# Kernel optimization log

Hardware: AMD Instinct MI355X
Metric: run time of the kernel (lower is better)

Reference implementation:

```python
import jax, jax.numpy as jnp
import numpy as np

IOU_THRES = 0.45
NEG_POS_RATIO = 3
BBOX_XFORM_CLIP = float(np.log(1000.0 / 16.0))  # torchvision BoxCoder clamp


def _make_boxes(key, shape, img=512.0):
    # valid xyxy boxes inside a 512x512 image
    k1, k2 = jax.random.split(key)
    cxy = jax.random.uniform(k1, shape + (2,), minval=32.0, maxval=img - 32.0)
    wh = jax.random.uniform(k2, shape + (2,), minval=8.0, maxval=128.0)
    return jnp.concatenate([cxy - 0.5 * wh, cxy + 0.5 * wh], axis=-1)


def setup_inputs() -> dict:
    key = jax.random.key(0)
    B, A, G, C = 32, 32768, 64, 91
    ks = jax.random.split(key, 5)
    return {
        "cls_logits": jax.random.normal(ks[0], (B, A, C), dtype=jnp.float32),
        "bbox_regression": 0.1 * jax.random.normal(ks[1], (B, A, 4), dtype=jnp.float32),
        "anchors": _make_boxes(ks[2], (B, A)),
        "gt_boxes": _make_boxes(ks[3], (B, G)),
        "gt_labels": jax.random.randint(ks[4], (B, G), 0, C - 1),  # fg classes; C-1 is background
    }


def _pairwise_iou(boxes, anchors):
    # boxes [B,G,4] xyxy, anchors [B,A,4] xyxy -> [B,G,A]
    b = boxes[:, :, None, :]
    a = anchors[:, None, :, :]
    tl = jnp.maximum(b[..., :2], a[..., :2])
    br = jnp.minimum(b[..., 2:], a[..., 2:])
    wh = jnp.clip(br - tl, 0.0)
    inter = wh[..., 0] * wh[..., 1]
    area_b = (b[..., 2] - b[..., 0]) * (b[..., 3] - b[..., 1])
    area_a = (a[..., 2] - a[..., 0]) * (a[..., 3] - a[..., 1])
    return inter / (area_b + area_a - inter + 1e-16)


def _match(ious):
    # SSDMatcher: per-anchor best gt, threshold, then force best anchor per gt.
    # ious [G,A] -> matches [A] in {-1, 0..G-1}
    G = ious.shape[0]
    vals = ious.max(axis=0)
    m = jnp.argmax(ious, axis=0)
    m = jnp.where(vals < IOU_THRES, -1, m)
    best_anchor_per_gt = jnp.argmax(ious, axis=1)  # [G]
    return m.at[best_anchor_per_gt].set(jnp.arange(G))


def _decode(reg, anchors):
    # torchvision BoxCoder.decode_single, weights (1,1,1,1), xyxy anchors
    w = anchors[..., 2] - anchors[..., 0]
    h = anchors[..., 3] - anchors[..., 1]
    cx = anchors[..., 0] + 0.5 * w
    cy = anchors[..., 1] + 0.5 * h
    dx, dy, dw, dh = reg[..., 0], reg[..., 1], reg[..., 2], reg[..., 3]
    dw = jnp.minimum(dw, BBOX_XFORM_CLIP)
    dh = jnp.minimum(dh, BBOX_XFORM_CLIP)
    pcx = dx * w + cx
    pcy = dy * h + cy
    pw = jnp.exp(dw) * w
    ph = jnp.exp(dh) * h
    return jnp.stack([pcx - 0.5 * pw, pcy - 0.5 * ph, pcx + 0.5 * pw, pcy + 0.5 * ph], axis=-1)


def _giou_loss(pred, gt):
    # GIoU loss on xyxy boxes; elementwise over leading dims
    tl = jnp.maximum(pred[..., :2], gt[..., :2])
    br = jnp.minimum(pred[..., 2:], gt[..., 2:])
    wh = jnp.clip(br - tl, 0.0)
    inter = wh[..., 0] * wh[..., 1]
    ap = (pred[..., 2] - pred[..., 0]) * (pred[..., 3] - pred[..., 1])
    ag = (gt[..., 2] - gt[..., 0]) * (gt[..., 3] - gt[..., 1])
    union = ap + ag - inter + 1e-16
    iou = inter / union
    ctl = jnp.minimum(pred[..., :2], gt[..., :2])
    cbr = jnp.maximum(pred[..., 2:], gt[..., 2:])
    cwh = cbr - ctl
    ac = cwh[..., 0] * cwh[..., 1]
    giou = iou - (ac - union) / jnp.clip(ac, 1e-16)
    return 1.0 - jnp.clip(giou, -1.0, 1.0)


def reference(cls_logits, bbox_regression, anchors, gt_boxes, gt_labels):
    B, A, C = cls_logits.shape
    # --- matching ---
    ious = _pairwise_iou(gt_boxes, anchors)        # [B,G,A]
    matched = jax.vmap(_match)(ious)               # [B,A]
    fg = matched >= 0                              # [B,A]
    idx = jnp.clip(matched, 0)
    num_fg = fg.sum()
    # --- bbox loss (sum over foreground only, via masking) ---
    matched_gt = jnp.take_along_axis(gt_boxes, idx[..., None], axis=1)  # [B,A,4]
    pred = _decode(bbox_regression, anchors)                            # [B,A,4]
    bbox_loss_sum = jnp.sum(_giou_loss(pred, matched_gt) * fg)
    # --- classification targets + CE ---
    matched_lbl = jnp.take_along_axis(gt_labels, idx, axis=1)           # [B,A]
    cls_targets = jnp.where(fg, matched_lbl, C - 1)
    logp = jax.nn.log_softmax(cls_logits, axis=-1)
    cls_loss = -jnp.take_along_axis(logp, cls_targets[..., None], axis=-1)[..., 0]  # [B,A]
    neg_loss = jnp.where(fg, -jnp.inf, cls_loss)
    order = jnp.argsort(-neg_loss, axis=1)         # descending
    rank = jnp.argsort(order, axis=1)
    num_neg = NEG_POS_RATIO * fg.sum(axis=1, keepdims=True)
    bg = rank < num_neg
    # --- normalize ---
    N = jnp.maximum(1, num_fg).astype(cls_loss.dtype)
    bbox_loss = 2.0 * bbox_loss_sum / N
    cls_total = (jnp.sum(cls_loss * fg) + jnp.sum(cls_loss * bg)) / N
    return jnp.stack([bbox_loss, cls_total])  # [bbox_loss, cls_loss]
```

## Files before the change

### kernel.cpp

```cpp
#include <hip/hip_runtime.h>
#include <hip/hip_bf16.h>

#define B 32
#define A 32768
#define G 64
#define C 91
#define NBINS 2048

typedef unsigned long long ull;

static constexpr size_t offMatched = 0;
static constexpr size_t offLoss    = (size_t)B * A * 4;
static constexpr size_t offHist    = (size_t)2 * B * A * 4;
static constexpr size_t offNumFg   = offHist + (size_t)B * NBINS * 4;
static constexpr size_t offPrefix  = offNumFg + B * 4;
static constexpr size_t offKrem    = offPrefix + B * 4;
static constexpr size_t offDone    = offKrem + B * 4;
static constexpr size_t offT       = offDone + B * 4;
static constexpr size_t offR       = offT + B * 4;
static constexpr size_t offAcc     = offR + B * 4;
static constexpr size_t offGt      = offAcc + 3 * 8;
static constexpr int    ZERO_N     = (int)((offGt - offHist) / 4);

__global__ void init_kernel(int* zero_base, ull* gtpack) {
  int i = blockIdx.x * 256 + threadIdx.x;
  for (int j = i; j < ZERO_N; j += gridDim.x * 256) zero_base[j] = 0;
  if (i < B * G) gtpack[i] = 0xFFFFFFFFull;
}

__global__ __launch_bounds__(256) void match_kernel(
    const float4* __restrict__ anchors, const float4* __restrict__ gt_boxes,
    int* __restrict__ matched, ull* __restrict__ gtpack) {
#pragma clang fp contract(off)
  int b = blockIdx.y;
  int a = blockIdx.x * 256 + threadIdx.x;
  __shared__ float4 gtb[G];
  __shared__ float gtarea[G];
  __shared__ ull best[G];
  if (threadIdx.x < G) {
    float4 g = gt_boxes[b * G + threadIdx.x];
    gtb[threadIdx.x] = g;
    gtarea[threadIdx.x] = (g.z - g.x) * (g.w - g.y);
    best[threadIdx.x] = 0ull;
  }
  __syncthreads();
  float4 an = anchors[(size_t)b * A + a];
  float area_a = (an.z - an.x) * (an.w - an.y);
  float bestv = -1.0f;
  int bestg = 0;
  for (int g = 0; g < G; ++g) {
    float4 gb = gtb[g];
    float tlx = fmaxf(gb.x, an.x), tly = fmaxf(gb.y, an.y);
    float brx = fminf(gb.z, an.z), bry = fminf(gb.w, an.w);
    float w = fmaxf(brx - tlx, 0.0f), h = fmaxf(bry - tly, 0.0f);
    float inter = w * h;
    float iou = 0.0f;
    if (inter > 0.0f) iou = inter / (gtarea[g] + area_a - inter + 1e-16f);
    if (iou > bestv) { bestv = iou; bestg = g; }
    if (iou > 0.0f) {
      ull p = ((ull)__float_as_uint(iou) << 32) | (unsigned)(~(unsigned)a);
      if (p > best[g]) atomicMax(&best[g], p);
    }
  }
  matched[(size_t)b * A + a] = (bestv < 0.45f) ? -1 : bestg;
  __syncthreads();
  if (threadIdx.x < G) {
    ull p = best[threadIdx.x];
    if (p) atomicMax(&gtpack[b * G + threadIdx.x], p);
  }
}

__global__ void force_kernel(const ull* __restrict__ gtpack, int* __restrict__ matched) {
  int b = blockIdx.x * blockDim.x + threadIdx.x;
  if (b < B) {
    for (int g = 0; g < G; ++g) {
      unsigned a = ~(unsigned)(gtpack[b * G + g] & 0xFFFFFFFFull);
      matched[(size_t)b * A + a] = g;
    }
  }
}

#define APB 64
#define NT 8
#define NF4 (APB * C / 4)
#define NSTG 6
#define TAILN (NF4 - (NSTG - 1) * 256)

__device__ __forceinline__ void stage_tile(const float4* src, float* dst, int tid) {
  int wbase = tid & ~63;
#pragma unroll
  for (int r = 0; r < NSTG - 1; ++r)
    __builtin_amdgcn_global_load_lds(
        (const __attribute__((address_space(1))) void*)(src + r * 256 + tid),
        (__attribute__((address_space(3))) void*)(dst + (r * 256 + wbase) * 4),
        16, 0, 0);
  if (tid < TAILN)
    __builtin_amdgcn_global_load_lds(
        (const __attribute__((address_space(1))) void*)(src + (NSTG - 1) * 256 + tid),
        (__attribute__((address_space(3))) void*)(dst + ((NSTG - 1) * 256 + wbase) * 4),
        16, 0, 0);
}

__global__ __launch_bounds__(256) void loss_kernel(
    const float4* __restrict__ logit4, const float4* __restrict__ reg,
    const float4* __restrict__ anchors, const float4* __restrict__ gt_boxes,
    const int* __restrict__ gt_labels, const int* __restrict__ matched,
    float* __restrict__ cls_loss, int* __restrict__ num_fg, double* __restrict__ acc) {
  __shared__ float buf[2][APB * C];
  __shared__ double rb[4], rf[4];
  __shared__ int rc[4];
  int tid = threadIdx.x;
  int b = blockIdx.y;
  int tile0 = blockIdx.x * NT;
  size_t bbase4 = (size_t)b * A * C / 4;
  int t4 = tid >> 2, q = tid & 3;

  stage_tile(logit4 + bbase4 + (size_t)tile0 * NF4, buf[0], tid);
  int mmCur = matched[(size_t)b * A + tile0 * APB + t4];
  int tclsCur = (mmCur >= 0) ? gt_labels[b * G + mmCur] : (C - 1);
  __syncthreads();

  double bbs = 0.0, fgs = 0.0;
  int cnt = 0;

  for (int t = 0; t < NT; ++t) {
    int cur = t & 1;
    if (t + 1 < NT)
      stage_tile(logit4 + bbase4 + (size_t)(tile0 + t + 1) * NF4, buf[cur ^ 1], tid);
    int mmNext = 0, tclsNext = 0;
    if (t + 1 < NT) {
      mmNext = matched[(size_t)b * A + (tile0 + t + 1) * APB + t4];
      tclsNext = (mmNext >= 0) ? gt_labels[b * G + mmNext] : (C - 1);
    }
    {
      const float* BC = buf[cur];
      int a = (tile0 + t) * APB + t4;
      const float* row = BC + t4 * C + 23 * q;
      const int cn = (q < 3) ? 23 : 22;
      float s0 = 0.f, s1 = 0.f, s2 = 0.f, s3 = 0.f;
      int j = 0;
#pragma unroll
      for (; j + 4 <= 20; j += 4) {
        s0 += __expf(row[j]);
        s1 += __expf(row[j + 1]);
        s2 += __expf(row[j + 2]);
        s3 += __expf(row[j + 3]);
      }
      for (; j < cn; ++j) s0 += __expf(row[j]);
      float s = (s0 + s1) + (s2 + s3);
      s += __shfl_xor(s, 1);
      s += __shfl_xor(s, 2);
      float lse = __logf(s);
      float xt = BC[t4 * C + tclsCur];
      float loss = lse - xt;
      if (q == 0) {
        cls_loss[(size_t)b * A + a] = loss;
        if (mmCur >= 0) {
          fgs += (double)loss;
          cnt++;
          float4 an = anchors[(size_t)b * A + a];
          float4 rg = reg[(size_t)b * A + a];
          float4 gb = gt_boxes[b * G + mmCur];
          float w = an.z - an.x, h = an.w - an.y;
          float cx = an.x + 0.5f * w, cy = an.y + 0.5f * h;
          float dw = fminf(rg.z, 4.135166556742356f);
          float dh = fminf(rg.w, 4.135166556742356f);
          float pcx = rg.x * w + cx, pcy = rg.y * h + cy;
          float pw = expf(dw) * w, ph = expf(dh) * h;
          float px0 = pcx - 0.5f * pw, py0 = pcy - 0.5f * ph;
          float px1 = pcx + 0.5f * pw, py1 = pcy + 0.5f * ph;
          float tlx = fmaxf(px0, gb.x), tly = fmaxf(py0, gb.y);
          float brx = fminf(px1, gb.z), bry = fminf(py1, gb.w);
          float iw = fmaxf(brx - tlx, 0.f), ih = fmaxf(bry - tly, 0.f);
          float inter = iw * ih;
          float ap = (px1 - px0) * (py1 - py0);
          float ag = (gb.z - gb.x) * (gb.w - gb.y);
          float uni = ap + ag - inter + 1e-16f;
          float iou = inter / uni;
          float ctlx = fminf(px0, gb.x), ctly = fminf(py0, gb.y);
          float cbrx = fmaxf(px1, gb.z), cbry = fmaxf(py1, gb.w);
          float acr = (cbrx - ctlx) * (cbry - ctly);
          float giou = iou - (acr - uni) / fmaxf(acr, 1e-16f);
          giou = fminf(fmaxf(giou, -1.f), 1.f);
          bbs += (double)(1.f - giou);
        }
      }
    }
    mmCur = mmNext;
    tclsCur = tclsNext;
    __syncthreads();
  }

  int lane = tid & 63, wave = tid >> 6;
  for (int off = 32; off; off >>= 1) {
    bbs += __shfl_xor(bbs, off);
    fgs += __shfl_xor(fgs, off);
    cnt += __shfl_xor(cnt, off);
  }
  if (lane == 0) { rb[wave] = bbs; rf[wave] = fgs; rc[wave] = cnt; }
  __syncthreads();
  if (tid == 0) {
    double tb = rb[0] + rb[1] + rb[2] + rb[3];
    double tf = rf[0] + rf[1] + rf[2] + rf[3];
    int tc = rc[0] + rc[1] + rc[2] + rc[3];
    if (tb != 0.0) atomicAdd(&acc[0], tb);
    if (tf != 0.0) atomicAdd(&acc[1], tf);
    if (tc) atomicAdd(&num_fg[b], tc);
  }
}

__global__ __launch_bounds__(256) void hist_kernel(
    const float* __restrict__ cls_loss, const int* __restrict__ matched,
    int* __restrict__ hist, const int* __restrict__ done,
    const unsigned* __restrict__ prefix, int level) {
  int b = blockIdx.y;
  if (level > 1 && done[b]) return;
  __shared__ int h[NBINS];
  for (int i = threadIdx.x; i < NBINS; i += 256) h[i] = 0;
  __syncthreads();
  unsigned pref = (level > 1) ? prefix[b] : 0u;
  int base = blockIdx.x * 2048;
  for (int i = 0; i < 8; ++i) {
    int a = base + i * 256 + threadIdx.x;
    if (matched[(size_t)b * A + a] < 0) {
      unsigned bits = __float_as_uint(cls_loss[(size_t)b * A + a]);
      if (level == 1) atomicAdd(&h[bits >> 21], 1);
      else if (level == 2) { if ((bits >> 21) == pref) atomicAdd(&h[(bits >> 10) & 2047], 1); }
      else { if ((bits >> 10) == pref) atomicAdd(&h[bits & 1023], 1); }
    }
  }
  __syncthreads();
  for (int i = threadIdx.x; i < NBINS; i += 256)
    if (h[i]) atomicAdd(&hist[b * NBINS + i], h[i]);
}

__global__ __launch_bounds__(256) void select_kernel(
    int* __restrict__ hist, const int* __restrict__ num_fg, int* __restrict__ done,
    unsigned* __restrict__ prefix, int* __restrict__ krem, float* __restrict__ T,
    int* __restrict__ r, double* __restrict__ acc, int level) {
  int b = blockIdx.x;
  if (level > 1 && done[b]) return;
  int nb = (level == 3) ? 1024 : 2048;
  int per = nb / 256;
  __shared__ int h[NBINS];
  __shared__ int gsum[256];
  for (int i = threadIdx.x; i < nb; i += 256) {
    h[i] = hist[b * NBINS + i];
    hist[b * NBINS + i] = 0;
  }
  __syncthreads();
  int gs = 0;
  for (int j = 0; j < per; ++j) gs += h[threadIdx.x * per + j];
  gsum[threadIdx.x] = gs;
  __syncthreads();
  if (threadIdx.x == 0) {
    int k;
    bool dn = false;
    if (level == 1) {
      int nf = num_fg[b];
      k = 3 * nf;
      int bgcnt = A - nf;
      if (k <= 0) { T[b] = __builtin_inff(); r[b] = 0; done[b] = 1; dn = true; }
      else if (k >= bgcnt) { T[b] = -1.0f; r[b] = 0; done[b] = 1; dn = true; }
    } else {
      k = krem[b];
    }
    if (!dn) {
      int run = 0, gidx = 255;
      for (; gidx >= 0; --gidx) {
        if (run + gsum[gidx] >= k) break;
        run += gsum[gidx];
      }
      if (gidx < 0) {
        T[b] = -1.0f; r[b] = 0; done[b] = 1;
      } else {
        int bin = gidx * per + per - 1;
        for (; bin > gidx * per; --bin) {
          if (run + h[bin] >= k) break;
          run += h[bin];
        }
        int kn = k - run;
        if (level == 1) { prefix[b] = (unsigned)bin; krem[b] = kn; }
        else if (level == 2) { prefix[b] = (prefix[b] << 11) | (unsigned)bin; krem[b] = kn; }
        else {
          unsigned bits = (prefix[b] << 10) | (unsigned)bin;
          float t = __uint_as_float(bits);
          T[b] = t; r[b] = kn;
          if (kn > 0) atomicAdd(&acc[2], (double)kn * (double)t);
        }
      }
    }
  }
}

__global__ __launch_bounds__(256) void bgsum_kernel(
    const float* __restrict__ cls_loss, const int* __restrict__ matched,
    const float* __restrict__ T, double* __restrict__ acc) {
  int b = blockIdx.y;
  float t = T[b];
  float local = 0.f;
  int base = blockIdx.x * 2048;
  for (int i = 0; i < 8; ++i) {
    int a = base + i * 256 + threadIdx.x;
    if (matched[(size_t)b * A + a] < 0) {
      float v = cls_loss[(size_t)b * A + a];
      if (v > t) local += v;
    }
  }
  for (int off = 32; off; off >>= 1) local += __shfl_xor(local, off);
  __shared__ double sd[4];
  if ((threadIdx.x & 63) == 0) sd[threadIdx.x >> 6] = (double)local;
  __syncthreads();
  if (threadIdx.x == 0) {
    double tt = sd[0] + sd[1] + sd[2] + sd[3];
    if (tt != 0.0) atomicAdd(&acc[2], tt);
  }
}

__global__ void finalize_kernel(const int* __restrict__ num_fg,
                                const double* __restrict__ acc, float* __restrict__ out) {
  if (threadIdx.x == 0 && blockIdx.x == 0) {
    int tot = 0;
    for (int b = 0; b < B; ++b) tot += num_fg[b];
    double N = (double)(tot > 1 ? tot : 1);
    out[0] = (float)(2.0 * acc[0] / N);
    out[1] = (float)((acc[1] + acc[2]) / N);
  }
}

extern "C" void kernel_launch(void* const* d_in, const int* in_sizes, int n_in,
                              void* d_out, int out_size, void* d_ws, size_t ws_size,
                              hipStream_t stream) {
  const float4* logit4  = (const float4*)d_in[0];
  const float4* reg     = (const float4*)d_in[1];
  const float4* anchors = (const float4*)d_in[2];
  const float4* gtb     = (const float4*)d_in[3];
  const int*    gtl     = (const int*)d_in[4];

  char* ws = (char*)d_ws;
  int*      matched = (int*)(ws + offMatched);
  float*    closs   = (float*)(ws + offLoss);
  int*      hist    = (int*)(ws + offHist);
  int*      numfg   = (int*)(ws + offNumFg);
  unsigned* prefix  = (unsigned*)(ws + offPrefix);
  int*      krem    = (int*)(ws + offKrem);
  int*      done    = (int*)(ws + offDone);
  float*    T       = (float*)(ws + offT);
  int*      r       = (int*)(ws + offR);
  double*   acc     = (double*)(ws + offAcc);
  ull*      gtpack  = (ull*)(ws + offGt);
  float*    out     = (float*)d_out;

  init_kernel<<<64, 256, 0, stream>>>((int*)(ws + offHist), gtpack);
  match_kernel<<<dim3(A / 256, B), 256, 0, stream>>>(anchors, gtb, matched, gtpack);
  force_kernel<<<1, 64, 0, stream>>>(gtpack, matched);
  loss_kernel<<<dim3(A / (APB * NT), B), 256, 0, stream>>>(
      logit4, reg, anchors, gtb, gtl, matched, closs, numfg, acc);
  hist_kernel<<<dim3(A / 2048, B), 256, 0, stream>>>(closs, matched, hist, done, prefix, 1);
  select_kernel<<<B, 256, 0, stream>>>(hist, numfg, done, prefix, krem, T, r, acc, 1);
  hist_kernel<<<dim3(A / 2048, B), 256, 0, stream>>>(closs, matched, hist, done, prefix, 2);
  select_kernel<<<B, 256, 0, stream>>>(hist, numfg, done, prefix, krem, T, r, acc, 2);
  hist_kernel<<<dim3(A / 2048, B), 256, 0, stream>>>(closs, matched, hist, done, prefix, 3);
  select_kernel<<<B, 256, 0, stream>>>(hist, numfg, done, prefix, krem, T, r, acc, 3);
  bgsum_kernel<<<dim3(A / 2048, B), 256, 0, stream>>>(closs, matched, T, acc);
  finalize_kernel<<<1, 64, 0, stream>>>(numfg, acc, out);
}
```

Baseline: 730.3 us.

## Fuse radix-select passes into one per-image kernel and fold the force and finalize steps

Replaces the three histogram and select kernel pairs, the background sum and the finalize kernel with a single kernel using one 1024-thread block per image. Each block holds all of that image's loss bits in registers and runs three radix histogram levels in shared memory. The forced-match step moves into the last match block, and finalize into the last select block, both coordinated by atomic tickets. The loss kernel now writes masked bits (zero for foreground), so the selection passes no longer re-read the match array. This trims kernel launches and global re-reads, in exchange for only 32 blocks in the select phase and reliance on threadfence and ticket ordering.

```diff
diff --git a/kernel.cpp b/kernel.cpp
--- a/kernel.cpp
+++ b/kernel.cpp
@@ -10,33 +10,29 @@
 typedef unsigned long long ull;
 
 static constexpr size_t offMatched = 0;
-static constexpr size_t offLoss    = (size_t)B * A * 4;
-static constexpr size_t offHist    = (size_t)2 * B * A * 4;
-static constexpr size_t offNumFg   = offHist + (size_t)B * NBINS * 4;
-static constexpr size_t offPrefix  = offNumFg + B * 4;
-static constexpr size_t offKrem    = offPrefix + B * 4;
-static constexpr size_t offDone    = offKrem + B * 4;
-static constexpr size_t offT       = offDone + B * 4;
-static constexpr size_t offR       = offT + B * 4;
-static constexpr size_t offAcc     = offR + B * 4;
-static constexpr size_t offGt      = offAcc + 3 * 8;
-static constexpr int    ZERO_N     = (int)((offGt - offHist) / 4);
+static constexpr size_t offBits    = (size_t)B * A * 4;
+static constexpr size_t offNumFg   = (size_t)2 * B * A * 4;
+static constexpr size_t offAcc     = offNumFg + B * 4;
+static constexpr size_t offTick    = offAcc + 3 * 8;
+static constexpr size_t offGt      = offTick + 8;
+static constexpr int    ZERO_N     = (int)((offGt - offNumFg) / 4);
 
 __global__ void init_kernel(int* zero_base, ull* gtpack) {
   int i = blockIdx.x * 256 + threadIdx.x;
-  for (int j = i; j < ZERO_N; j += gridDim.x * 256) zero_base[j] = 0;
+  if (i < ZERO_N) zero_base[i] = 0;
   if (i < B * G) gtpack[i] = 0xFFFFFFFFull;
 }
 
 __global__ __launch_bounds__(256) void match_kernel(
     const float4* __restrict__ anchors, const float4* __restrict__ gt_boxes,
-    int* __restrict__ matched, ull* __restrict__ gtpack) {
+    int* __restrict__ matched, ull* __restrict__ gtpack, int* __restrict__ ticket) {
 #pragma clang fp contract(off)
   int b = blockIdx.y;
   int a = blockIdx.x * 256 + threadIdx.x;
   __shared__ float4 gtb[G];
   __shared__ float gtarea[G];
   __shared__ ull best[G];
+  __shared__ int lastBlk;
   if (threadIdx.x < G) {
     float4 g = gt_boxes[b * G + threadIdx.x];
     gtb[threadIdx.x] = g;
@@ -68,14 +64,17 @@
     ull p = best[threadIdx.x];
     if (p) atomicMax(&gtpack[b * G + threadIdx.x], p);
   }
-}
-
-__global__ void force_kernel(const ull* __restrict__ gtpack, int* __restrict__ matched) {
-  int b = blockIdx.x * blockDim.x + threadIdx.x;
-  if (b < B) {
+  __threadfence();
+  __syncthreads();
+  if (threadIdx.x == 0)
+    lastBlk = (atomicAdd(ticket, 1) == (int)(gridDim.x * gridDim.y) - 1);
+  __syncthreads();
+  if (lastBlk && threadIdx.x < B) {
+    int bb = threadIdx.x;
     for (int g = 0; g < G; ++g) {
-      unsigned a = ~(unsigned)(gtpack[b * G + g] & 0xFFFFFFFFull);
-      matched[(size_t)b * A + a] = g;
+      ull p = atomicAdd(&gtpack[bb * G + g], 0ull);
+      unsigned aa = ~(unsigned)(p & 0xFFFFFFFFull);
+      matched[(size_t)bb * A + aa] = g;
     }
   }
 }
@@ -105,7 +104,7 @@
     const float4* __restrict__ logit4, const float4* __restrict__ reg,
     const float4* __restrict__ anchors, const float4* __restrict__ gt_boxes,
     const int* __restrict__ gt_labels, const int* __restrict__ matched,
-    float* __restrict__ cls_loss, int* __restrict__ num_fg, double* __restrict__ acc) {
+    unsigned* __restrict__ cls_bits, int* __restrict__ num_fg, double* __restrict__ acc) {
   __shared__ float buf[2][APB * C];
   __shared__ double rb[4], rf[4];
   __shared__ int rc[4];
@@ -154,7 +153,7 @@
       float xt = BC[t4 * C + tclsCur];
       float loss = lse - xt;
       if (q == 0) {
-        cls_loss[(size_t)b * A + a] = loss;
+        cls_bits[(size_t)b * A + a] = (mmCur >= 0) ? 0u : __float_as_uint(loss);
         if (mmCur >= 0) {
           fgs += (double)loss;
           cnt++;
@@ -209,122 +208,137 @@
   }
 }
 
-__global__ __launch_bounds__(256) void hist_kernel(
-    const float* __restrict__ cls_loss, const int* __restrict__ matched,
-    int* __restrict__ hist, const int* __restrict__ done,
-    const unsigned* __restrict__ prefix, int level) {
-  int b = blockIdx.y;
-  if (level > 1 && done[b]) return;
-  __shared__ int h[NBINS];
-  for (int i = threadIdx.x; i < NBINS; i += 256) h[i] = 0;
-  __syncthreads();
-  unsigned pref = (level > 1) ? prefix[b] : 0u;
-  int base = blockIdx.x * 2048;
-  for (int i = 0; i < 8; ++i) {
-    int a = base + i * 256 + threadIdx.x;
-    if (matched[(size_t)b * A + a] < 0) {
-      unsigned bits = __float_as_uint(cls_loss[(size_t)b * A + a]);
-      if (level == 1) atomicAdd(&h[bits >> 21], 1);
-      else if (level == 2) { if ((bits >> 21) == pref) atomicAdd(&h[(bits >> 10) & 2047], 1); }
-      else { if ((bits >> 10) == pref) atomicAdd(&h[bits & 1023], 1); }
-    }
-  }
-  __syncthreads();
-  for (int i = threadIdx.x; i < NBINS; i += 256)
-    if (h[i]) atomicAdd(&hist[b * NBINS + i], h[i]);
-}
-
-__global__ __launch_bounds__(256) void select_kernel(
-    int* __restrict__ hist, const int* __restrict__ num_fg, int* __restrict__ done,
-    unsigned* __restrict__ prefix, int* __restrict__ krem, float* __restrict__ T,
-    int* __restrict__ r, double* __restrict__ acc, int level) {
-  int b = blockIdx.x;
-  if (level > 1 && done[b]) return;
-  int nb = (level == 3) ? 1024 : 2048;
-  int per = nb / 256;
+__global__ __launch_bounds__(1024) void select_fused(
+    const unsigned* __restrict__ bits, const int* __restrict__ num_fg,
+    double* __restrict__ acc, int* __restrict__ ticket, float* __restrict__ out) {
+  int b = blockIdx.x, tid = threadIdx.x;
   __shared__ int h[NBINS];
   __shared__ int gsum[256];
-  for (int i = threadIdx.x; i < nb; i += 256) {
-    h[i] = hist[b * NBINS + i];
-    hist[b * NBINS + i] = 0;
-  }
-  __syncthreads();
-  int gs = 0;
-  for (int j = 0; j < per; ++j) gs += h[threadIdx.x * per + j];
-  gsum[threadIdx.x] = gs;
-  __syncthreads();
-  if (threadIdx.x == 0) {
-    int k;
-    bool dn = false;
-    if (level == 1) {
-      int nf = num_fg[b];
-      k = 3 * nf;
-      int bgcnt = A - nf;
-      if (k <= 0) { T[b] = __builtin_inff(); r[b] = 0; done[b] = 1; dn = true; }
-      else if (k >= bgcnt) { T[b] = -1.0f; r[b] = 0; done[b] = 1; dn = true; }
-    } else {
-      k = krem[b];
-    }
-    if (!dn) {
+  __shared__ float sT;
+  __shared__ int sDone, sKrem, sR;
+  __shared__ unsigned sPref;
+  __shared__ double sd[16];
+
+  unsigned bv[32];
+#pragma unroll
+  for (int i = 0; i < 32; ++i) bv[i] = bits[(size_t)b * A + i * 1024 + tid];
+  if (tid == 0) { sDone = 0; sR = 0; }
+
+  for (int i = tid; i < NBINS; i += 1024) h[i] = 0;
+  __syncthreads();
+#pragma unroll
+  for (int i = 0; i < 32; ++i) atomicAdd(&h[bv[i] >> 21], 1);
+  __syncthreads();
+  if (tid < 256) {
+    int gs = 0;
+#pragma unroll
+    for (int j = 0; j < 8; ++j) gs += h[tid * 8 + j];
+    gsum[tid] = gs;
+  }
+  __syncthreads();
+  if (tid == 0) {
+    int nf = num_fg[b];
+    int k = 3 * nf;
+    int bgcnt = A - nf;
+    if (k <= 0) { sT = __builtin_inff(); sDone = 1; }
+    else if (k >= bgcnt) { sT = -1.0f; sDone = 1; }
+    else {
       int run = 0, gidx = 255;
-      for (; gidx >= 0; --gidx) {
-        if (run + gsum[gidx] >= k) break;
-        run += gsum[gidx];
-      }
-      if (gidx < 0) {
-        T[b] = -1.0f; r[b] = 0; done[b] = 1;
-      } else {
-        int bin = gidx * per + per - 1;
-        for (; bin > gidx * per; --bin) {
-          if (run + h[bin] >= k) break;
-          run += h[bin];
-        }
-        int kn = k - run;
-        if (level == 1) { prefix[b] = (unsigned)bin; krem[b] = kn; }
-        else if (level == 2) { prefix[b] = (prefix[b] << 11) | (unsigned)bin; krem[b] = kn; }
-        else {
-          unsigned bits = (prefix[b] << 10) | (unsigned)bin;
-          float t = __uint_as_float(bits);
-          T[b] = t; r[b] = kn;
-          if (kn > 0) atomicAdd(&acc[2], (double)kn * (double)t);
-        }
-      }
-    }
-  }
-}
-
-__global__ __launch_bounds__(256) void bgsum_kernel(
-    const float* __restrict__ cls_loss, const int* __restrict__ matched,
-    const float* __restrict__ T, double* __restrict__ acc) {
-  int b = blockIdx.y;
-  float t = T[b];
-  float local = 0.f;
-  int base = blockIdx.x * 2048;
-  for (int i = 0; i < 8; ++i) {
-    int a = base + i * 256 + threadIdx.x;
-    if (matched[(size_t)b * A + a] < 0) {
-      float v = cls_loss[(size_t)b * A + a];
-      if (v > t) local += v;
-    }
-  }
-  for (int off = 32; off; off >>= 1) local += __shfl_xor(local, off);
-  __shared__ double sd[4];
-  if ((threadIdx.x & 63) == 0) sd[threadIdx.x >> 6] = (double)local;
-  __syncthreads();
-  if (threadIdx.x == 0) {
-    double tt = sd[0] + sd[1] + sd[2] + sd[3];
+      for (; gidx >= 0; --gidx) { if (run + gsum[gidx] >= k) break; run += gsum[gidx]; }
+      if (gidx < 0) { sT = -1.0f; sDone = 1; }
+      else {
+        int bin = gidx * 8 + 7;
+        for (; bin > gidx * 8; --bin) { if (run + h[bin] >= k) break; run += h[bin]; }
+        sPref = (unsigned)bin; sKrem = k - run;
+      }
+    }
+  }
+  __syncthreads();
+
+  if (!sDone) {
+    unsigned p1 = sPref;
+    int k = sKrem;
+    __syncthreads();
+    for (int i = tid; i < NBINS; i += 1024) h[i] = 0;
+    __syncthreads();
+#pragma unroll
+    for (int i = 0; i < 32; ++i)
+      if ((bv[i] >> 21) == p1) atomicAdd(&h[(bv[i] >> 10) & 2047], 1);
+    __syncthreads();
+    if (tid < 256) {
+      int gs = 0;
+#pragma unroll
+      for (int j = 0; j < 8; ++j) gs += h[tid * 8 + j];
+      gsum[tid] = gs;
+    }
+    __syncthreads();
+    if (tid == 0) {
+      int run = 0, gidx = 255;
+      for (; gidx >= 0; --gidx) { if (run + gsum[gidx] >= k) break; run += gsum[gidx]; }
+      if (gidx < 0) { sT = -1.0f; sDone = 1; }
+      else {
+        int bin = gidx * 8 + 7;
+        for (; bin > gidx * 8; --bin) { if (run + h[bin] >= k) break; run += h[bin]; }
+        sPref = (p1 << 11) | (unsigned)bin; sKrem = k - run;
+      }
+    }
+    __syncthreads();
+  }
+  if (!sDone) {
+    unsigned p2 = sPref;
+    int k = sKrem;
+    __syncthreads();
+    if (tid < 1024) h[tid] = 0;
+    __syncthreads();
+#pragma unroll
+    for (int i = 0; i < 32; ++i)
+      if ((bv[i] >> 10) == p2) atomicAdd(&h[bv[i] & 1023], 1);
+    __syncthreads();
+    if (tid < 256) {
+      int gs = 0;
+#pragma unroll
+      for (int j = 0; j < 4; ++j) gs += h[tid * 4 + j];
+      gsum[tid] = gs;
+    }
+    __syncthreads();
+    if (tid == 0) {
+      int run = 0, gidx = 255;
+      for (; gidx >= 0; --gidx) { if (run + gsum[gidx] >= k) break; run += gsum[gidx]; }
+      if (gidx < 0) { sT = -1.0f; }
+      else {
+        int bin = gidx * 4 + 3;
+        for (; bin > gidx * 4; --bin) { if (run + h[bin] >= k) break; run += h[bin]; }
+        sT = __uint_as_float((p2 << 10) | (unsigned)bin);
+        sR = k - run;
+      }
+    }
+    __syncthreads();
+  }
+
+  float T = sT;
+  float ls = 0.f;
+#pragma unroll
+  for (int i = 0; i < 32; ++i) {
+    float v = __uint_as_float(bv[i]);
+    if (v > T) ls += v;
+  }
+  for (int off = 32; off; off >>= 1) ls += __shfl_xor(ls, off);
+  if ((tid & 63) == 0) sd[tid >> 6] = (double)ls;
+  __syncthreads();
+  if (tid == 0) {
+    double tt = 0.0;
+    for (int w = 0; w < 16; ++w) tt += sd[w];
+    if (sR > 0) tt += (double)sR * (double)sT;
     if (tt != 0.0) atomicAdd(&acc[2], tt);
-  }
-}
-
-__global__ void finalize_kernel(const int* __restrict__ num_fg,
-                                const double* __restrict__ acc, float* __restrict__ out) {
-  if (threadIdx.x == 0 && blockIdx.x == 0) {
-    int tot = 0;
-    for (int b = 0; b < B; ++b) tot += num_fg[b];
-    double N = (double)(tot > 1 ? tot : 1);
-    out[0] = (float)(2.0 * acc[0] / N);
-    out[1] = (float)((acc[1] + acc[2]) / N);
+    __threadfence();
+    if (atomicAdd(ticket, 1) == B - 1) {
+      int tot = 0;
+      for (int bb = 0; bb < B; ++bb) tot += num_fg[bb];
+      double N = (double)(tot > 1 ? tot : 1);
+      double a2 = atomicAdd(&acc[2], 0.0);
+      out[0] = (float)(2.0 * acc[0] / N);
+      out[1] = (float)((acc[1] + a2) / N);
+    }
   }
 }
 
@@ -339,29 +353,16 @@
 
   char* ws = (char*)d_ws;
   int*      matched = (int*)(ws + offMatched);
-  float*    closs   = (float*)(ws + offLoss);
-  int*      hist    = (int*)(ws + offHist);
+  unsigned* cbits   = (unsigned*)(ws + offBits);
   int*      numfg   = (int*)(ws + offNumFg);
-  unsigned* prefix  = (unsigned*)(ws + offPrefix);
-  int*      krem    = (int*)(ws + offKrem);
-  int*      done    = (int*)(ws + offDone);
-  float*    T       = (float*)(ws + offT);
-  int*      r       = (int*)(ws + offR);
   double*   acc     = (double*)(ws + offAcc);
+  int*      tick    = (int*)(ws + offTick);
   ull*      gtpack  = (ull*)(ws + offGt);
   float*    out     = (float*)d_out;
 
-  init_kernel<<<64, 256, 0, stream>>>((int*)(ws + offHist), gtpack);
-  match_kernel<<<dim3(A / 256, B), 256, 0, stream>>>(anchors, gtb, matched, gtpack);
-  force_kernel<<<1, 64, 0, stream>>>(gtpack, matched);
+  init_kernel<<<8, 256, 0, stream>>>((int*)(ws + offNumFg), gtpack);
+  match_kernel<<<dim3(A / 256, B), 256, 0, stream>>>(anchors, gtb, matched, gtpack, tick);
   loss_kernel<<<dim3(A / (APB * NT), B), 256, 0, stream>>>(
-      logit4, reg, anchors, gtb, gtl, matched, closs, numfg, acc);
-  hist_kernel<<<dim3(A / 2048, B), 256, 0, stream>>>(closs, matched, hist, done, prefix, 1);
-  select_kernel<<<B, 256, 0, stream>>>(hist, numfg, done, prefix, krem, T, r, acc, 1);
-  hist_kernel<<<dim3(A / 2048, B), 256, 0, stream>>>(closs, matched, hist, done, prefix, 2);
-  select_kernel<<<B, 256, 0, stream>>>(hist, numfg, done, prefix, krem, T, r, acc, 2);
-  hist_kernel<<<dim3(A / 2048, B), 256, 0, stream>>>(closs, matched, hist, done, prefix, 3);
-  select_kernel<<<B, 256, 0, stream>>>(hist, numfg, done, prefix, krem, T, r, acc, 3);
-  bgsum_kernel<<<dim3(A / 2048, B), 256, 0, stream>>>(closs, matched, T, acc);
-  finalize_kernel<<<1, 64, 0, stream>>>(numfg, acc, out);
-}
+      logit4, reg, anchors, gtb, gtl, matched, cbits, numfg, acc);
+  select_fused<<<B, 1024, 0, stream>>>(cbits, numfg, acc, tick + 1, out);
+}
```

After: 895.7 us. 22.7% more time.
